# Optimization experiments

Hardware: AMD Instinct MI355X
Metric: run time of the kernel (lower is better)

## Reference

```python
import jax, jax.numpy as jnp
import numpy as np

NUM_EXPERTS = 2
TOP_K = 2


def setup_inputs() -> dict:
    key = jax.random.key(0)
    ks = jax.random.split(key, 5)
    B, T, M, H, E = 8, 512, 2048, 1024, NUM_EXPERTS
    x = jax.random.normal(ks[0], (B, T, M), dtype=jnp.float32)
    wg = jax.random.normal(ks[1], (M, E), dtype=jnp.float32) * 0.02
    w1 = jax.random.normal(ks[2], (E, M, H), dtype=jnp.float32) * 0.02
    b1 = jnp.zeros((E, H), dtype=jnp.float32)
    w2 = jax.random.normal(ks[3], (E, H, M), dtype=jnp.float32) * 0.02
    b2 = jnp.zeros((E, M), dtype=jnp.float32)
    return {"x": x, "wg": wg, "w1": w1, "b1": b1, "w2": w2, "b2": b2}


def _moe_forward(x, wg, w1, b1, w2, b2):
    B, T, M = x.shape
    E = wg.shape[1]
    S = B * T
    C = TOP_K * ((S + E - 1) // E)  # GShard top-2 capacity, factor 1.0
    xf = x.reshape(S, M)

    # --- fp32 gate (Top2Gate) ---
    logits = jnp.einsum('sm,me->se', xf.astype(jnp.float32), wg.astype(jnp.float32))
    gates = jax.nn.softmax(logits, axis=-1)  # [S,E]

    idx1 = jnp.argmax(gates, axis=-1)
    mask1 = jax.nn.one_hot(idx1, E, dtype=jnp.float32)
    gates_wo1 = jnp.where(mask1 > 0, -jnp.inf, logits)
    idx2 = jnp.argmax(gates_wo1, axis=-1)
    mask2 = jax.nn.one_hot(idx2, E, dtype=jnp.float32)

    # positions within each expert's buffer
    loc1 = jnp.cumsum(mask1, axis=0) - 1.0                      # [S,E]
    loc2 = jnp.cumsum(mask2, axis=0) - 1.0 + jnp.sum(mask1, axis=0, keepdims=True)
    mask1 = mask1 * (loc1 < C)
    mask2 = mask2 * (loc2 < C)

    g1 = jnp.sum(gates * mask1, axis=1)  # [S]
    g2 = jnp.sum(gates * mask2, axis=1)
    denom = jnp.maximum(g1 + g2, jnp.finfo(jnp.float32).eps)
    g1, g2 = g1 / denom, g2 / denom

    p1 = jnp.sum(loc1 * mask1, axis=1).astype(jnp.int32)  # capacity slot per token
    p2 = jnp.sum(loc2 * mask2, axis=1).astype(jnp.int32)
    oh1 = jax.nn.one_hot(p1, C, dtype=jnp.float32)  # [S,C]
    oh2 = jax.nn.one_hot(p2, C, dtype=jnp.float32)

    combine = (g1[:, None, None] * mask1[:, :, None] * oh1[:, None, :]
               + g2[:, None, None] * mask2[:, :, None] * oh2[:, None, :])  # [S,E,C]
    dispatch = (combine > 0).astype(xf.dtype)

    # --- dispatch, grouped expert FFN, combine ---
    disp = jnp.einsum('sec,sm->ecm', dispatch, xf)                 # [E,C,M]
    h = jax.nn.relu(jnp.einsum('ecm,emh->ech', disp, w1) + b1[:, None, :])
    y = jnp.einsum('ech,ehm->ecm', h, w2) + b2[:, None, :]         # [E,C,M]
    out = jnp.einsum('sec,ecm->sm', combine.astype(xf.dtype), y)   # [S,M]
    return out.reshape(B, T, M)


def reference(x, wg, w1, b1, w2, b2):
    moe_out = _moe_forward(x, wg, w1, b1, w2, b2)          # [B,T,M]
    summed = jnp.sum(moe_out, axis=2)                      # [B,T]
    return jax.nn.log_softmax(summed, axis=1)
```

## Files before the change

kernel.cpp:

```cpp
#include <hip/hip_runtime.h>

typedef unsigned short u16;
typedef unsigned int   u32;
typedef u16   u16x4 __attribute__((ext_vector_type(4)));
typedef u16   u16x8 __attribute__((ext_vector_type(8)));
typedef short s16x8 __attribute__((ext_vector_type(8)));
typedef float f32x4 __attribute__((ext_vector_type(4)));

#define S_TOK 4096
#define MDIM  2048
#define NDIM  2048
#define HDIM  1024
#define TDIM  512

__device__ __forceinline__ u16 f2bf(float f) {
  u32 u = __float_as_uint(f);
  u = u + 0x7fffu + ((u >> 16) & 1u);
  return (u16)(u >> 16);
}

__device__ __forceinline__ void gl2lds16(const void* g, void* l) {
  __builtin_amdgcn_global_load_lds(
      (const __attribute__((address_space(1))) void*)g,
      (__attribute__((address_space(3))) void*)l, 16, 0, 0);
}

__global__ __launch_bounds__(256) void prep_w1t(const float* __restrict__ w1,
                                                u16* __restrict__ w1t) {
  __shared__ float tile[32][33];
  int bid = blockIdx.x;
  int e   = bid >> 11;
  int idx = bid & 2047;
  int m0  = (idx >> 5) << 5;
  int h0  = (idx & 31) << 5;
  int t = threadIdx.x;
  int r = t >> 3, q = t & 7;
  const float* src = w1 + ((size_t)e * MDIM + (m0 + r)) * HDIM + h0 + q * 4;
  f32x4 v = *(const f32x4*)src;
  tile[r][q*4+0] = v[0]; tile[r][q*4+1] = v[1];
  tile[r][q*4+2] = v[2]; tile[r][q*4+3] = v[3];
  __syncthreads();
  u16x4 o;
  o[0] = f2bf(tile[q*4+0][r]);
  o[1] = f2bf(tile[q*4+1][r]);
  o[2] = f2bf(tile[q*4+2][r]);
  o[3] = f2bf(tile[q*4+3][r]);
  u16* dst = w1t + ((size_t)e * HDIM + (h0 + r)) * MDIM + m0 + q * 4;
  *(u16x4*)dst = o;
}

__global__ __launch_bounds__(256) void prep_sums(const float* __restrict__ w2,
                                                 const float* __restrict__ b2,
                                                 float* __restrict__ w2sum,
                                                 float* __restrict__ b2sum) {
  int row  = blockIdx.x * 4 + (threadIdx.x >> 6);
  int lane = threadIdx.x & 63;
  const float* src;
  if (row < NDIM)          src = w2 + (size_t)row * MDIM;
  else if (row < NDIM + 2) src = b2 + (size_t)(row - NDIM) * MDIM;
  else return;
  float acc = 0.f;
  for (int m = lane * 4; m < MDIM; m += 256) {
    f32x4 v = *(const f32x4*)(src + m);
    acc += v[0] + v[1] + v[2] + v[3];
  }
  #pragma unroll
  for (int off = 32; off; off >>= 1) acc += __shfl_xor(acc, off);
  if (lane == 0) {
    if (row < NDIM) w2sum[row] = acc;
    else            b2sum[row - NDIM] = acc;
  }
}

__global__ __launch_bounds__(256) void gate_xbf(const float* __restrict__ x,
                                                const float* __restrict__ wg,
                                                float* __restrict__ g,
                                                u16* __restrict__ xbf) {
  int s    = blockIdx.x * 4 + (threadIdx.x >> 6);
  int lane = threadIdx.x & 63;
  const float* xr = x + (size_t)s * MDIM;
  u16* xbr = xbf + (size_t)s * MDIM;
  float l0 = 0.f, l1 = 0.f;
  for (int m = lane * 4; m < MDIM; m += 256) {
    f32x4 xv = *(const f32x4*)(xr + m);
    f32x4 wa = *(const f32x4*)(wg + 2 * m);
    f32x4 wb = *(const f32x4*)(wg + 2 * m + 4);
    l0 += xv[0]*wa[0] + xv[1]*wa[2] + xv[2]*wb[0] + xv[3]*wb[2];
    l1 += xv[0]*wa[1] + xv[1]*wa[3] + xv[2]*wb[1] + xv[3]*wb[3];
    u16x4 o; o[0]=f2bf(xv[0]); o[1]=f2bf(xv[1]); o[2]=f2bf(xv[2]); o[3]=f2bf(xv[3]);
    *(u16x4*)(xbr + m) = o;
  }
  #pragma unroll
  for (int off = 32; off; off >>= 1) {
    l0 += __shfl_xor(l0, off);
    l1 += __shfl_xor(l1, off);
  }
  if (lane == 0) {
    float mx = fmaxf(l0, l1);
    float e0 = expf(l0 - mx), e1 = expf(l1 - mx);
    float inv = 1.f / (e0 + e1);
    g[2*s]   = e0 * inv;
    g[2*s+1] = e1 * inv;
  }
}

#define BM 128
#define BN 128
#define BK 64
#define KT (MDIM / BK)

__global__ __launch_bounds__(512, 4) void gemm_fused(const u16* __restrict__ xbf,
                                                     const u16* __restrict__ w1t,
                                                     const float* __restrict__ b1,
                                                     const float* __restrict__ w2sum,
                                                     float* __restrict__ ssum) {
  __shared__ u16 As[2][BM * BK];
  __shared__ u16 Bs[2][BN * BK];

  int bid  = blockIdx.x;
  int tile = (bid & 7) * 64 + (bid >> 3);
  int bn = tile & 15;
  int bm = tile >> 4;
  int gs0 = bm * BM;
  int gn0 = bn * BN;

  int tid  = threadIdx.x;
  int lane = tid & 63;
  int wid  = tid >> 6;
  int wr = wid >> 2, wc = wid & 3;
  int fr = lane & 15, fg = lane >> 4;

  int lr = lane >> 3;
  int lc = (lane & 7) ^ lr;
  int row0 = wid * 16;
  const u16* asrc = xbf + (size_t)(gs0 + row0 + lr) * MDIM + lc * 8;
  const u16* bsrc = w1t + (size_t)(gn0 + row0 + lr) * MDIM + lc * 8;

  f32x4 acc[4][2] = {};

  {
    gl2lds16(asrc,            &As[0][ row0      * BK]);
    gl2lds16(asrc + 8 * MDIM, &As[0][(row0 + 8) * BK]);
    gl2lds16(bsrc,            &Bs[0][ row0      * BK]);
    gl2lds16(bsrc + 8 * MDIM, &Bs[0][(row0 + 8) * BK]);
  }

  for (int kt = 0; kt < KT; ++kt) {
    int cur = kt & 1;
    __syncthreads();
    if (kt + 1 < KT) {
      int k0 = (kt + 1) * BK;
      gl2lds16(asrc + k0,            &As[cur ^ 1][ row0      * BK]);
      gl2lds16(asrc + k0 + 8 * MDIM, &As[cur ^ 1][(row0 + 8) * BK]);
      gl2lds16(bsrc + k0,            &Bs[cur ^ 1][ row0      * BK]);
      gl2lds16(bsrc + k0 + 8 * MDIM, &Bs[cur ^ 1][(row0 + 8) * BK]);
    }
    #pragma unroll
    for (int kk = 0; kk < 2; ++kk) {
      s16x8 af[4], bfr[2];
      #pragma unroll
      for (int i = 0; i < 4; ++i) {
        int row = wr * 64 + i * 16 + fr;
        int ch  = (fg + 4 * kk) ^ (fr & 7);
        af[i] = *(const s16x8*)(&As[cur][row * BK + ch * 8]);
      }
      #pragma unroll
      for (int j = 0; j < 2; ++j) {
        int row = wc * 32 + j * 16 + fr;
        int ch  = (fg + 4 * kk) ^ (fr & 7);
        bfr[j] = *(const s16x8*)(&Bs[cur][row * BK + ch * 8]);
      }
      #pragma unroll
      for (int i = 0; i < 4; ++i)
        #pragma unroll
        for (int j = 0; j < 2; ++j)
          acc[i][j] = __builtin_amdgcn_mfma_f32_16x16x32_bf16(af[i], bfr[j], acc[i][j], 0, 0, 0);
    }
  }

  int e = gn0 >> 10;
  float b1v[2], w2v[2];
  #pragma unroll
  for (int j = 0; j < 2; ++j) {
    int n = gn0 + wc * 32 + j * 16 + fr;
    b1v[j] = b1[n];
    w2v[j] = w2sum[n];
  }
  #pragma unroll
  for (int i = 0; i < 4; ++i) {
    #pragma unroll
    for (int r = 0; r < 4; ++r) {
      float sv = 0.f;
      #pragma unroll
      for (int j = 0; j < 2; ++j)
        sv += fmaxf(acc[i][j][r] + b1v[j], 0.f) * w2v[j];
      sv += __shfl_xor(sv, 1);
      sv += __shfl_xor(sv, 2);
      sv += __shfl_xor(sv, 4);
      sv += __shfl_xor(sv, 8);
      if (fr == 0) {
        int s = gs0 + wr * 64 + i * 16 + fg * 4 + r;
        atomicAdd(&ssum[(size_t)e * S_TOK + s], sv);
      }
    }
  }
}

__global__ __launch_bounds__(512) void finalize(const float* __restrict__ g,
                                                const float* __restrict__ ssum,
                                                const float* __restrict__ b2sum,
                                                float* __restrict__ out) {
  __shared__ float sA[8];
  __shared__ float sB[2];
  int b = blockIdx.x;
  int t = threadIdx.x;
  int s = b * TDIM + t;
  int lane = t & 63, wid = t >> 6;
  float g0 = g[2*s], g1 = g[2*s+1];
  float v = g0 * (ssum[s] + b2sum[0]) + g1 * (ssum[S_TOK + s] + b2sum[1]);
  float m = v;
  #pragma unroll
  for (int off = 32; off; off >>= 1) m = fmaxf(m, __shfl_xor(m, off));
  if (lane == 0) sA[wid] = m;
  __syncthreads();
  if (t == 0) {
    float mm = sA[0];
    #pragma unroll
    for (int i = 1; i < 8; ++i) mm = fmaxf(mm, sA[i]);
    sB[0] = mm;
  }
  __syncthreads();
  float gm = sB[0];
  float ex = expf(v - gm);
  float sum = ex;
  #pragma unroll
  for (int off = 32; off; off >>= 1) sum += __shfl_xor(sum, off);
  if (lane == 0) sA[wid] = sum;
  __syncthreads();
  if (t == 0) {
    float ss = 0.f;
    #pragma unroll
    for (int i = 0; i < 8; ++i) ss += sA[i];
    sB[1] = logf(ss);
  }
  __syncthreads();
  out[s] = v - gm - sB[1];
}

extern "C" void kernel_launch(void* const* d_in, const int* in_sizes, int n_in,
                              void* d_out, int out_size, void* d_ws, size_t ws_size,
                              hipStream_t stream) {
  const float* x  = (const float*)d_in[0];
  const float* wg = (const float*)d_in[1];
  const float* w1 = (const float*)d_in[2];
  const float* b1 = (const float*)d_in[3];
  const float* w2 = (const float*)d_in[4];
  const float* b2 = (const float*)d_in[5];
  float* out = (float*)d_out;

  char* ws = (char*)d_ws;
  u16*   w1t   = (u16*)ws;
  u16*   xbf   = (u16*)(ws + 8388608);
  float* ssum  = (float*)(ws + 25165824);
  float* gbuf  = (float*)(ws + 25198592);
  float* w2sum = (float*)(ws + 25231360);
  float* b2sum = (float*)(ws + 25239552);

  hipMemsetAsync(ssum, 0, S_TOK * 2 * sizeof(float), stream);
  hipLaunchKernelGGL(prep_w1t,   dim3(4096), dim3(256), 0, stream, w1, w1t);
  hipLaunchKernelGGL(prep_sums,  dim3(513),  dim3(256), 0, stream, w2, b2, w2sum, b2sum);
  hipLaunchKernelGGL(gate_xbf,   dim3(1024), dim3(256), 0, stream, x, wg, gbuf, xbf);
  hipLaunchKernelGGL(gemm_fused, dim3(512),  dim3(512), 0, stream, xbf, w1t, b1, w2sum, ssum);
  hipLaunchKernelGGL(finalize,   dim3(8),    dim3(512), 0, stream, gbuf, ssum, b2sum, out);
}
```

Before: 69.53 us.

## Merge prep kernels into one launch and widen GEMM tile with direct-register A loads

Folds the three preprocessing kernels into a single launch that dispatches on block index, removing two kernel launches and their serialization gaps. The fused GEMM widens its N tile from 128 to 256 and halves the grid. It no longer stages the A operand (x in bf16) through LDS; each wave loads its A fragments straight from global memory into registers and prefetches the next k-step during the MFMAs. This cuts LDS traffic and raises MFMA work per B-tile load, at the cost of more registers per thread, uncoalesced global A reads and only 256 blocks to fill the GPU.

```diff
diff --git a/kernel.cpp b/kernel.cpp
--- a/kernel.cpp
+++ b/kernel.cpp
@@ -25,102 +25,105 @@
       (__attribute__((address_space(3))) void*)l, 16, 0, 0);
 }
 
-__global__ __launch_bounds__(256) void prep_w1t(const float* __restrict__ w1,
-                                                u16* __restrict__ w1t) {
-  __shared__ float tile[32][33];
-  int bid = blockIdx.x;
-  int e   = bid >> 11;
-  int idx = bid & 2047;
-  int m0  = (idx >> 5) << 5;
-  int h0  = (idx & 31) << 5;
-  int t = threadIdx.x;
-  int r = t >> 3, q = t & 7;
-  const float* src = w1 + ((size_t)e * MDIM + (m0 + r)) * HDIM + h0 + q * 4;
-  f32x4 v = *(const f32x4*)src;
-  tile[r][q*4+0] = v[0]; tile[r][q*4+1] = v[1];
-  tile[r][q*4+2] = v[2]; tile[r][q*4+3] = v[3];
-  __syncthreads();
-  u16x4 o;
-  o[0] = f2bf(tile[q*4+0][r]);
-  o[1] = f2bf(tile[q*4+1][r]);
-  o[2] = f2bf(tile[q*4+2][r]);
-  o[3] = f2bf(tile[q*4+3][r]);
-  u16* dst = w1t + ((size_t)e * HDIM + (h0 + r)) * MDIM + m0 + q * 4;
-  *(u16x4*)dst = o;
-}
-
-__global__ __launch_bounds__(256) void prep_sums(const float* __restrict__ w2,
-                                                 const float* __restrict__ b2,
-                                                 float* __restrict__ w2sum,
-                                                 float* __restrict__ b2sum) {
-  int row  = blockIdx.x * 4 + (threadIdx.x >> 6);
-  int lane = threadIdx.x & 63;
-  const float* src;
-  if (row < NDIM)          src = w2 + (size_t)row * MDIM;
-  else if (row < NDIM + 2) src = b2 + (size_t)(row - NDIM) * MDIM;
-  else return;
-  float acc = 0.f;
-  for (int m = lane * 4; m < MDIM; m += 256) {
-    f32x4 v = *(const f32x4*)(src + m);
-    acc += v[0] + v[1] + v[2] + v[3];
-  }
-  #pragma unroll
-  for (int off = 32; off; off >>= 1) acc += __shfl_xor(acc, off);
-  if (lane == 0) {
-    if (row < NDIM) w2sum[row] = acc;
-    else            b2sum[row - NDIM] = acc;
-  }
-}
-
-__global__ __launch_bounds__(256) void gate_xbf(const float* __restrict__ x,
+__global__ __launch_bounds__(256) void prep_all(const float* __restrict__ w1,
+                                                u16* __restrict__ w1t,
+                                                const float* __restrict__ w2,
+                                                const float* __restrict__ b2,
+                                                float* __restrict__ w2sum,
+                                                float* __restrict__ b2sum,
+                                                const float* __restrict__ x,
                                                 const float* __restrict__ wg,
                                                 float* __restrict__ g,
                                                 u16* __restrict__ xbf) {
-  int s    = blockIdx.x * 4 + (threadIdx.x >> 6);
-  int lane = threadIdx.x & 63;
-  const float* xr = x + (size_t)s * MDIM;
-  u16* xbr = xbf + (size_t)s * MDIM;
-  float l0 = 0.f, l1 = 0.f;
-  for (int m = lane * 4; m < MDIM; m += 256) {
-    f32x4 xv = *(const f32x4*)(xr + m);
-    f32x4 wa = *(const f32x4*)(wg + 2 * m);
-    f32x4 wb = *(const f32x4*)(wg + 2 * m + 4);
-    l0 += xv[0]*wa[0] + xv[1]*wa[2] + xv[2]*wb[0] + xv[3]*wb[2];
-    l1 += xv[0]*wa[1] + xv[1]*wa[3] + xv[2]*wb[1] + xv[3]*wb[3];
-    u16x4 o; o[0]=f2bf(xv[0]); o[1]=f2bf(xv[1]); o[2]=f2bf(xv[2]); o[3]=f2bf(xv[3]);
-    *(u16x4*)(xbr + m) = o;
-  }
-  #pragma unroll
-  for (int off = 32; off; off >>= 1) {
-    l0 += __shfl_xor(l0, off);
-    l1 += __shfl_xor(l1, off);
-  }
-  if (lane == 0) {
-    float mx = fmaxf(l0, l1);
-    float e0 = expf(l0 - mx), e1 = expf(l1 - mx);
-    float inv = 1.f / (e0 + e1);
-    g[2*s]   = e0 * inv;
-    g[2*s+1] = e1 * inv;
+  __shared__ float tile[32][33];
+  int b = blockIdx.x;
+  int t = threadIdx.x;
+  if (b < 4096) {
+    int e   = b >> 11;
+    int idx = b & 2047;
+    int m0  = (idx >> 5) << 5;
+    int h0  = (idx & 31) << 5;
+    int r = t >> 3, q = t & 7;
+    const float* src = w1 + ((size_t)e * MDIM + (m0 + r)) * HDIM + h0 + q * 4;
+    f32x4 v = *(const f32x4*)src;
+    tile[r][q*4+0] = v[0]; tile[r][q*4+1] = v[1];
+    tile[r][q*4+2] = v[2]; tile[r][q*4+3] = v[3];
+    __syncthreads();
+    u16x4 o;
+    o[0] = f2bf(tile[q*4+0][r]);
+    o[1] = f2bf(tile[q*4+1][r]);
+    o[2] = f2bf(tile[q*4+2][r]);
+    o[3] = f2bf(tile[q*4+3][r]);
+    u16* dst = w1t + ((size_t)e * HDIM + (h0 + r)) * MDIM + m0 + q * 4;
+    *(u16x4*)dst = o;
+  } else if (b < 4609) {
+    int bid  = b - 4096;
+    int row  = bid * 4 + (t >> 6);
+    int lane = t & 63;
+    const float* src;
+    if (row < NDIM)          src = w2 + (size_t)row * MDIM;
+    else if (row < NDIM + 2) src = b2 + (size_t)(row - NDIM) * MDIM;
+    else return;
+    float acc = 0.f;
+    for (int m = lane * 4; m < MDIM; m += 256) {
+      f32x4 v = *(const f32x4*)(src + m);
+      acc += v[0] + v[1] + v[2] + v[3];
+    }
+    #pragma unroll
+    for (int off = 32; off; off >>= 1) acc += __shfl_xor(acc, off);
+    if (lane == 0) {
+      if (row < NDIM) w2sum[row] = acc;
+      else            b2sum[row - NDIM] = acc;
+    }
+  } else {
+    int bid  = b - 4609;
+    int s    = bid * 4 + (t >> 6);
+    int lane = t & 63;
+    const float* xr = x + (size_t)s * MDIM;
+    u16* xbr = xbf + (size_t)s * MDIM;
+    float l0 = 0.f, l1 = 0.f;
+    for (int m = lane * 4; m < MDIM; m += 256) {
+      f32x4 xv = *(const f32x4*)(xr + m);
+      f32x4 wa = *(const f32x4*)(wg + 2 * m);
+      f32x4 wb = *(const f32x4*)(wg + 2 * m + 4);
+      l0 += xv[0]*wa[0] + xv[1]*wa[2] + xv[2]*wb[0] + xv[3]*wb[2];
+      l1 += xv[0]*wa[1] + xv[1]*wa[3] + xv[2]*wb[1] + xv[3]*wb[3];
+      u16x4 o; o[0]=f2bf(xv[0]); o[1]=f2bf(xv[1]); o[2]=f2bf(xv[2]); o[3]=f2bf(xv[3]);
+      *(u16x4*)(xbr + m) = o;
+    }
+    #pragma unroll
+    for (int off = 32; off; off >>= 1) {
+      l0 += __shfl_xor(l0, off);
+      l1 += __shfl_xor(l1, off);
+    }
+    if (lane == 0) {
+      float mx = fmaxf(l0, l1);
+      float e0 = expf(l0 - mx), e1 = expf(l1 - mx);
+      float inv = 1.f / (e0 + e1);
+      g[2*s]   = e0 * inv;
+      g[2*s+1] = e1 * inv;
+    }
   }
 }
 
 #define BM 128
-#define BN 128
+#define BN 256
 #define BK 64
 #define KT (MDIM / BK)
+
+#define MFMA_BF16 __builtin_amdgcn_mfma_f32_16x16x32_bf16
 
 __global__ __launch_bounds__(512, 4) void gemm_fused(const u16* __restrict__ xbf,
                                                      const u16* __restrict__ w1t,
                                                      const float* __restrict__ b1,
                                                      const float* __restrict__ w2sum,
                                                      float* __restrict__ ssum) {
-  __shared__ u16 As[2][BM * BK];
   __shared__ u16 Bs[2][BN * BK];
 
   int bid  = blockIdx.x;
-  int tile = (bid & 7) * 64 + (bid >> 3);
-  int bn = tile & 15;
-  int bm = tile >> 4;
+  int tile = (bid & 7) * 32 + (bid >> 3);
+  int bm = tile >> 3;
+  int bn = tile & 7;
   int gs0 = bm * BM;
   int gn0 = bn * BN;
 
@@ -132,57 +135,80 @@
 
   int lr = lane >> 3;
   int lc = (lane & 7) ^ lr;
-  int row0 = wid * 16;
-  const u16* asrc = xbf + (size_t)(gs0 + row0 + lr) * MDIM + lc * 8;
-  const u16* bsrc = w1t + (size_t)(gn0 + row0 + lr) * MDIM + lc * 8;
-
-  f32x4 acc[4][2] = {};
-
-  {
-    gl2lds16(asrc,            &As[0][ row0      * BK]);
-    gl2lds16(asrc + 8 * MDIM, &As[0][(row0 + 8) * BK]);
-    gl2lds16(bsrc,            &Bs[0][ row0      * BK]);
-    gl2lds16(bsrc + 8 * MDIM, &Bs[0][(row0 + 8) * BK]);
-  }
-
-  for (int kt = 0; kt < KT; ++kt) {
-    int cur = kt & 1;
-    __syncthreads();
-    if (kt + 1 < KT) {
-      int k0 = (kt + 1) * BK;
-      gl2lds16(asrc + k0,            &As[cur ^ 1][ row0      * BK]);
-      gl2lds16(asrc + k0 + 8 * MDIM, &As[cur ^ 1][(row0 + 8) * BK]);
-      gl2lds16(bsrc + k0,            &Bs[cur ^ 1][ row0      * BK]);
-      gl2lds16(bsrc + k0 + 8 * MDIM, &Bs[cur ^ 1][(row0 + 8) * BK]);
-    }
-    #pragma unroll
-    for (int kk = 0; kk < 2; ++kk) {
-      s16x8 af[4], bfr[2];
-      #pragma unroll
-      for (int i = 0; i < 4; ++i) {
-        int row = wr * 64 + i * 16 + fr;
-        int ch  = (fg + 4 * kk) ^ (fr & 7);
-        af[i] = *(const s16x8*)(&As[cur][row * BK + ch * 8]);
-      }
-      #pragma unroll
-      for (int j = 0; j < 2; ++j) {
-        int row = wc * 32 + j * 16 + fr;
-        int ch  = (fg + 4 * kk) ^ (fr & 7);
-        bfr[j] = *(const s16x8*)(&Bs[cur][row * BK + ch * 8]);
-      }
+  const u16* bS = w1t + (size_t)(gn0 + wid * 32 + lr) * MDIM + lc * 8;
+  int bD = (wid * 32) * BK;
+
+  int ch0 = (fg ^ (fr & 7)) * 8;
+  int bOff[4];
+  #pragma unroll
+  for (int j = 0; j < 4; ++j) bOff[j] = (wc * 64 + j * 16 + fr) * BK + ch0;
+
+  const u16* aB = xbf + (size_t)(gs0 + wr * 64 + fr) * MDIM + fg * 8;
+
+  f32x4 acc[4][4] = {};
+  s16x8 ae[4], ao[4];
+
+  #pragma unroll
+  for (int q = 0; q < 4; ++q)
+    gl2lds16(bS + q * 8 * MDIM, &Bs[0][bD + q * 8 * BK]);
+  #pragma unroll
+  for (int i = 0; i < 4; ++i) ae[i] = *(const s16x8*)(aB + (size_t)i * 16 * MDIM);
+  #pragma unroll
+  for (int i = 0; i < 4; ++i) ao[i] = *(const s16x8*)(aB + (size_t)i * 16 * MDIM + 32);
+  __syncthreads();
+
+  for (int t = 0; t < KT; ++t) {
+    const u16* Bc = &Bs[t & 1][0];
+    u16* Bnx = &Bs[(t & 1) ^ 1][0];
+    bool notlast = (t + 1 < KT);
+    int nk = (t + 1) * BK;
+
+    if (notlast) {
+      #pragma unroll
+      for (int q = 0; q < 4; ++q)
+        gl2lds16(bS + nk + q * 8 * MDIM, Bnx + bD + q * 8 * BK);
+    }
+
+    {
+      s16x8 bf0[4];
+      #pragma unroll
+      for (int j = 0; j < 4; ++j) bf0[j] = *(const s16x8*)(Bc + bOff[j]);
       #pragma unroll
       for (int i = 0; i < 4; ++i)
         #pragma unroll
-        for (int j = 0; j < 2; ++j)
-          acc[i][j] = __builtin_amdgcn_mfma_f32_16x16x32_bf16(af[i], bfr[j], acc[i][j], 0, 0, 0);
-    }
+        for (int j = 0; j < 4; ++j)
+          acc[i][j] = MFMA_BF16(ae[i], bf0[j], acc[i][j], 0, 0, 0);
+    }
+    if (notlast) {
+      #pragma unroll
+      for (int i = 0; i < 4; ++i)
+        ae[i] = *(const s16x8*)(aB + (size_t)i * 16 * MDIM + nk);
+    }
+
+    {
+      s16x8 bf1[4];
+      #pragma unroll
+      for (int j = 0; j < 4; ++j) bf1[j] = *(const s16x8*)(Bc + (bOff[j] ^ 32));
+      #pragma unroll
+      for (int i = 0; i < 4; ++i)
+        #pragma unroll
+        for (int j = 0; j < 4; ++j)
+          acc[i][j] = MFMA_BF16(ao[i], bf1[j], acc[i][j], 0, 0, 0);
+    }
+    if (notlast) {
+      #pragma unroll
+      for (int i = 0; i < 4; ++i)
+        ao[i] = *(const s16x8*)(aB + (size_t)i * 16 * MDIM + nk + 32);
+    }
+
+    __syncthreads();
   }
 
   int e = gn0 >> 10;
-  float b1v[2], w2v[2];
-  #pragma unroll
-  for (int j = 0; j < 2; ++j) {
-    int n = gn0 + wc * 32 + j * 16 + fr;
+  float b1v[4], w2v[4];
+  #pragma unroll
+  for (int j = 0; j < 4; ++j) {
+    int n = gn0 + wc * 64 + j * 16 + fr;
     b1v[j] = b1[n];
     w2v[j] = w2sum[n];
   }
@@ -192,7 +218,7 @@
     for (int r = 0; r < 4; ++r) {
       float sv = 0.f;
       #pragma unroll
-      for (int j = 0; j < 2; ++j)
+      for (int j = 0; j < 4; ++j)
         sv += fmaxf(acc[i][j][r] + b1v[j], 0.f) * w2v[j];
       sv += __shfl_xor(sv, 1);
       sv += __shfl_xor(sv, 2);
@@ -267,9 +293,8 @@
   float* b2sum = (float*)(ws + 25239552);
 
   hipMemsetAsync(ssum, 0, S_TOK * 2 * sizeof(float), stream);
-  hipLaunchKernelGGL(prep_w1t,   dim3(4096), dim3(256), 0, stream, w1, w1t);
-  hipLaunchKernelGGL(prep_sums,  dim3(513),  dim3(256), 0, stream, w2, b2, w2sum, b2sum);
-  hipLaunchKernelGGL(gate_xbf,   dim3(1024), dim3(256), 0, stream, x, wg, gbuf, xbf);
-  hipLaunchKernelGGL(gemm_fused, dim3(512),  dim3(512), 0, stream, xbf, w1t, b1, w2sum, ssum);
+  hipLaunchKernelGGL(prep_all,   dim3(5633), dim3(256), 0, stream,
+                     w1, w1t, w2, b2, w2sum, b2sum, x, wg, gbuf, xbf);
+  hipLaunchKernelGGL(gemm_fused, dim3(256),  dim3(512), 0, stream, xbf, w1t, b1, w2sum, ssum);
   hipLaunchKernelGGL(finalize,   dim3(8),    dim3(512), 0, stream, gbuf, ssum, b2sum, out);
 }
```

New measurement: 112.7 us. 62.1% more time.
